# Optimization experiments

Hardware: AMD Instinct MI355X
Metric: run time of the kernel (lower is better)

The kernel has to match this reference:

```python
import jax, jax.numpy as jnp
import numpy as np

B, CQ, CK, CV, CO = 16, 256, 256, 256, 256
H, W = 80, 80          # query spatial size (P3-like)
KH, KW = 40, 40        # key/value spatial size (P4-like)
HEADS = 4
R2 = 2 * 2             # region_size ** 2
SCALE = 1.0 / np.float32(np.sqrt(CQ))


def conv1x1(x, w, b):
    # 1x1 conv == per-pixel linear map over channels
    return jnp.einsum('bchw,oc->bohw', x, w) + b[None, :, None, None]


def setup_inputs() -> dict:
    key = jax.random.key(0)
    ks = jax.random.split(key, 10)
    s = 0.05
    return {
        'query': jax.random.normal(ks[0], (B, CQ, H, W), jnp.float32),
        'key':   jax.random.normal(ks[1], (B, CK, KH, KW), jnp.float32),
        'wq': jax.random.normal(ks[2], (CQ, CQ), jnp.float32) * s,
        'bq': jax.random.normal(ks[3], (CQ,), jnp.float32) * s,
        'wk': jax.random.normal(ks[4], (CK, CK), jnp.float32) * s,
        'bk': jax.random.normal(ks[5], (CK,), jnp.float32) * s,
        'wv': jax.random.normal(ks[6], (CV, CV), jnp.float32) * s,
        'bv': jax.random.normal(ks[7], (CV,), jnp.float32) * s,
        'wo': jax.random.normal(ks[8], (CO, CV), jnp.float32) * s,
        'bo': jax.random.normal(ks[9], (CO,), jnp.float32) * s,
    }


def reference(query, key, wq, bq, wk, bk, wv, bv, wo, bo):
    # value defaults to key in the original module
    q = conv1x1(query, wq, bq)               # [B,CQ,H,W]
    k = conv1x1(key, wk, bk)                 # [B,CK,KH,KW]
    v = conv1x1(key, wv, bv)                 # [B,CV,KH,KW]

    b, cq, h, w = q.shape
    # All R2 'patches' in the source are the SAME interpolation (no offsets),
    # so compute it once; bilinear resize matches torch align_corners=False.
    ki = jax.image.resize(k, (b, k.shape[1], h, w), method='bilinear')
    vi = jax.image.resize(v, (b, v.shape[1], h, w), method='bilinear')

    q5 = q.reshape(b, HEADS, cq // HEADS, h, w)
    k5 = ki.reshape(b, HEADS, k.shape[1] // HEADS, h, w)
    v5 = vi.reshape(b, HEADS, v.shape[1] // HEADS, h, w)

    # per-region score; identical for every region patch
    score = jnp.einsum('bhcxy,bhcxy->bhxy', q5, k5) * SCALE     # [B,h,H,W]
    scores = jnp.broadcast_to(score[:, :, None], (b, HEADS, R2, h, w))
    # NOTE: original uses nn.Softmax(dim=3) -> normalizes over the H axis
    attn = jax.nn.softmax(scores, axis=3)                       # [B,h,R2,H,W]

    # out = sum over regions of attn * v (v identical across regions)
    out = jnp.einsum('bhrxy,bhcxy->bhcxy', attn, v5)            # [B,h,C/h,H,W]
    out = out.reshape(b, -1, h, w)                              # [B,CV,H,W]
    return conv1x1(out, wo, bo)                                 # [B,CO,H,W]
```

## Files before the change

kernel.cpp:

```cpp
#include <hip/hip_runtime.h>
#include <hip/hip_bf16.h>

typedef __bf16 bf16;
typedef __attribute__((ext_vector_type(4))) float f32x4;
typedef __attribute__((ext_vector_type(8))) __bf16 bf16x8;
typedef __attribute__((ext_vector_type(4))) __bf16 bf16x4;

static __device__ __forceinline__ void gl16(const void* g, void* l) {
  __builtin_amdgcn_global_load_lds((const __attribute__((address_space(1))) void*)g,
                                   (__attribute__((address_space(3))) void*)l, 16, 0, 0);
}
static __device__ __forceinline__ bf16x8 frag(const bf16* tile, int row, int kb) {
  return *(const bf16x8*)(tile + row * 64 + ((((kb) >> 3) ^ (row & 7)) << 3));
}

__global__ void wpre(const float* __restrict__ w0, const float* __restrict__ w1,
                     const float* __restrict__ w2, const float* __restrict__ w3,
                     bf16* __restrict__ dst) {
  const float* srcs[4] = {w0, w1, w2, w3};
  const float* s = srcs[blockIdx.y];
  bf16* d = dst + (size_t)blockIdx.y * 65536;
  int base = blockIdx.x * 2048 + threadIdx.x * 8;
  f32x4 a = *(const f32x4*)(s + base);
  f32x4 b = *(const f32x4*)(s + base + 4);
  bf16x8 v = {(bf16)a[0], (bf16)a[1], (bf16)a[2], (bf16)a[3],
              (bf16)b[0], (bf16)b[1], (bf16)b[2], (bf16)b[3]};
  *(bf16x8*)(d + base) = v;
}

__global__ __launch_bounds__(512, 1)
void qgemm_score(const float* __restrict__ query, const bf16* __restrict__ Wq,
                 const float* __restrict__ bq, const bf16* __restrict__ Kpm,
                 float* __restrict__ score) {
  __shared__ alignas(16) char smem[65536];
  const int t = threadIdx.x;
  const int b = blockIdx.z;
  const int m0 = blockIdx.x * 128;
  const int n0 = blockIdx.y * 128;
  const int w = t >> 6, l = t & 63;
  const int wr = w & 1, wc = w >> 1;
  const int lrow = l & 15, koff = (l >> 4) * 8;
  const int up = t & 31, uk = t >> 5;
  const float* actb = query + (size_t)b * 256 * 6400;

  f32x4 Ar[4];
  f32x4 acc[4][2];
#pragma unroll
  for (int i = 0; i < 4; ++i)
#pragma unroll
    for (int j = 0; j < 2; ++j) acc[i][j] = (f32x4){0.f, 0.f, 0.f, 0.f};

  auto Ab = [&](int buf) { return (bf16*)(smem + buf * 16384); };
  auto Bb = [&](int buf) { return (bf16*)(smem + 32768 + buf * 16384); };

  auto GLOADB = [&](int kt, int buf) {
    const int k0 = kt * 64;
#pragma unroll
    for (int call = 0; call < 2; ++call) {
      int idx = call * 512 + t;
      int row = idx >> 3, u = idx & 7;
      gl16(Wq + (size_t)(n0 + row) * 256 + k0 + ((u ^ (row & 7)) << 3), Bb(buf) + idx * 8);
    }
  };
  auto ALOAD = [&](int kt) {
    const int k0 = kt * 64;
    int ps = m0 + up * 4;
#pragma unroll
    for (int j = 0; j < 4; ++j)
      Ar[j] = *(const f32x4*)(actb + (size_t)(k0 + uk * 4 + j) * 6400 + ps);
  };
  auto ASTORE = [&](int buf) {
#pragma unroll
    for (int j = 0; j < 4; ++j) {
      int row = up * 4 + j;
      int cs = (uk * 4) ^ ((row & 7) << 3);
      bf16x4 v = {(bf16)Ar[0][j], (bf16)Ar[1][j], (bf16)Ar[2][j], (bf16)Ar[3][j]};
      *(bf16x4*)(Ab(buf) + row * 64 + cs) = v;
    }
  };
  auto COMPUTE = [&](int buf) {
#pragma unroll
    for (int kk = 0; kk < 2; ++kk) {
      const int kb = kk * 32 + koff;
      bf16x8 af[4], bv[2];
#pragma unroll
      for (int i = 0; i < 4; ++i) af[i] = frag(Ab(buf), wr * 64 + i * 16 + lrow, kb);
#pragma unroll
      for (int j = 0; j < 2; ++j) bv[j] = frag(Bb(buf), wc * 32 + j * 16 + lrow, kb);
#pragma unroll
      for (int i = 0; i < 4; ++i)
#pragma unroll
        for (int j = 0; j < 2; ++j)
          acc[i][j] = __builtin_amdgcn_mfma_f32_16x16x32_bf16(af[i], bv[j], acc[i][j], 0, 0, 0);
    }
  };

  GLOADB(0, 0);
  ALOAD(0);
  ASTORE(0);
  __syncthreads();
#pragma unroll
  for (int kt = 0; kt < 4; ++kt) {
    const int cur = kt & 1;
    if (kt < 3) { GLOADB(kt + 1, cur ^ 1); ALOAD(kt + 1); }
    __builtin_amdgcn_sched_barrier(0);
    COMPUTE(cur);
    if (kt < 3) ASTORE(cur ^ 1);
    __syncthreads();
  }

  bf16* Qs = (bf16*)smem;
#pragma unroll
  for (int mi = 0; mi < 4; ++mi) {
#pragma unroll
    for (int ni = 0; ni < 2; ++ni) {
      int ch = wc * 32 + ni * 16 + (l & 15);
      float bvf = bq[n0 + ch];
#pragma unroll
      for (int r = 0; r < 4; ++r) {
        int p = wr * 64 + mi * 16 + (l >> 4) * 4 + r;
        Qs[p * 136 + ch] = (bf16)(acc[mi][ni][r] + bvf);
      }
    }
  }
  __syncthreads();

  if (t < 256) {
    int pl = t & 127, hl = t >> 7;
    int hd = (n0 >> 6) + hl;
    int p = m0 + pl;
    int x = p / 80, y = p % 80;
    float cx = 0.5f * x - 0.25f;
    int ix = (int)floorf(cx);
    float wx1 = cx - ix;
    int x0 = ix < 0 ? 0 : ix, x1 = (ix + 1 > 39) ? 39 : ix + 1;
    float cy = 0.5f * y - 0.25f;
    int iy = (int)floorf(cy);
    float wy1 = cy - iy;
    int y0 = iy < 0 ? 0 : iy, y1 = (iy + 1 > 39) ? 39 : iy + 1;
    float w00 = (1.f - wx1) * (1.f - wy1), w01 = (1.f - wx1) * wy1;
    float w10 = wx1 * (1.f - wy1), w11 = wx1 * wy1;
    const bf16* k00 = Kpm + ((size_t)b * 1600 + x0 * 40 + y0) * 256 + hd * 64;
    const bf16* k01 = Kpm + ((size_t)b * 1600 + x0 * 40 + y1) * 256 + hd * 64;
    const bf16* k10 = Kpm + ((size_t)b * 1600 + x1 * 40 + y0) * 256 + hd * 64;
    const bf16* k11 = Kpm + ((size_t)b * 1600 + x1 * 40 + y1) * 256 + hd * 64;
    float dot = 0.f;
#pragma unroll
    for (int i = 0; i < 8; ++i) {
      bf16x8 qv = *(const bf16x8*)(Qs + pl * 136 + hl * 64 + i * 8);
      bf16x8 a = *(const bf16x8*)(k00 + i * 8);
      bf16x8 c = *(const bf16x8*)(k01 + i * 8);
      bf16x8 d = *(const bf16x8*)(k10 + i * 8);
      bf16x8 e = *(const bf16x8*)(k11 + i * 8);
#pragma unroll
      for (int j = 0; j < 8; ++j) {
        float kup = w00 * (float)a[j] + w01 * (float)c[j] + w10 * (float)d[j] + w11 * (float)e[j];
        dot += (float)qv[j] * kup;
      }
    }
    score[((size_t)b * 4 + hd) * 6400 + p] = dot * 0.0625f;
  }
}

__global__ __launch_bounds__(512, 1)
void kv_gemm(const float* __restrict__ key,
             const bf16* __restrict__ Wk, const float* __restrict__ bk, bf16* __restrict__ Kpm,
             const bf16* __restrict__ Wv, const float* __restrict__ bv, bf16* __restrict__ Vpm) {
  __shared__ alignas(16) char smem[65536];
  const int P = 1600;
  const int t = threadIdx.x;
  const int b = blockIdx.z;
  const int m0 = blockIdx.x * 128;
  const int sel = blockIdx.y >> 1;
  const int n0 = (blockIdx.y & 1) * 128;
  const bf16* W = sel ? Wv : Wk;
  const float* bias = sel ? bv : bk;
  bf16* out = sel ? Vpm : Kpm;
  const int w = t >> 6, l = t & 63;
  const int wr = w & 1, wc = w >> 1;
  const int lrow = l & 15, koff = (l >> 4) * 8;
  const int up = t & 31, uk = t >> 5;
  const float* actb = key + (size_t)b * 256 * P;

  f32x4 Ar[4];
  f32x4 acc[4][2];
#pragma unroll
  for (int i = 0; i < 4; ++i)
#pragma unroll
    for (int j = 0; j < 2; ++j) acc[i][j] = (f32x4){0.f, 0.f, 0.f, 0.f};

  auto Ab = [&](int buf) { return (bf16*)(smem + buf * 16384); };
  auto Bb = [&](int buf) { return (bf16*)(smem + 32768 + buf * 16384); };

  auto GLOADB = [&](int kt, int buf) {
    const int k0 = kt * 64;
#pragma unroll
    for (int call = 0; call < 2; ++call) {
      int idx = call * 512 + t;
      int row = idx >> 3, u = idx & 7;
      gl16(W + (size_t)(n0 + row) * 256 + k0 + ((u ^ (row & 7)) << 3), Bb(buf) + idx * 8);
    }
  };
  auto ALOAD = [&](int kt) {
    const int k0 = kt * 64;
    int ps = m0 + up * 4;
    if (ps > P - 4) ps = P - 4;
#pragma unroll
    for (int j = 0; j < 4; ++j)
      Ar[j] = *(const f32x4*)(actb + (size_t)(k0 + uk * 4 + j) * P + ps);
  };
  auto ASTORE = [&](int buf) {
#pragma unroll
    for (int j = 0; j < 4; ++j) {
      int row = up * 4 + j;
      int cs = (uk * 4) ^ ((row & 7) << 3);
      bf16x4 v = {(bf16)Ar[0][j], (bf16)Ar[1][j], (bf16)Ar[2][j], (bf16)Ar[3][j]};
      *(bf16x4*)(Ab(buf) + row * 64 + cs) = v;
    }
  };
  auto COMPUTE = [&](int buf) {
#pragma unroll
    for (int kk = 0; kk < 2; ++kk) {
      const int kb = kk * 32 + koff;
      bf16x8 af[4], bvv[2];
#pragma unroll
      for (int i = 0; i < 4; ++i) af[i] = frag(Ab(buf), wr * 64 + i * 16 + lrow, kb);
#pragma unroll
      for (int j = 0; j < 2; ++j) bvv[j] = frag(Bb(buf), wc * 32 + j * 16 + lrow, kb);
#pragma unroll
      for (int i = 0; i < 4; ++i)
#pragma unroll
        for (int j = 0; j < 2; ++j)
          acc[i][j] = __builtin_amdgcn_mfma_f32_16x16x32_bf16(af[i], bvv[j], acc[i][j], 0, 0, 0);
    }
  };

  GLOADB(0, 0);
  ALOAD(0);
  ASTORE(0);
  __syncthreads();
#pragma unroll
  for (int kt = 0; kt < 4; ++kt) {
    const int cur = kt & 1;
    if (kt < 3) { GLOADB(kt + 1, cur ^ 1); ALOAD(kt + 1); }
    __builtin_amdgcn_sched_barrier(0);
    COMPUTE(cur);
    if (kt < 3) ASTORE(cur ^ 1);
    __syncthreads();
  }

  bf16* Sc = (bf16*)smem;
#pragma unroll
  for (int mi = 0; mi < 4; ++mi) {
#pragma unroll
    for (int ni = 0; ni < 2; ++ni) {
      int ch = wc * 32 + ni * 16 + (l & 15);
      float bvf = bias[n0 + ch];
#pragma unroll
      for (int r = 0; r < 4; ++r) {
        int p = wr * 64 + mi * 16 + (l >> 4) * 4 + r;
        Sc[p * 136 + ch] = (bf16)(acc[mi][ni][r] + bvf);
      }
    }
  }
  __syncthreads();
  bf16* ob = out + (size_t)b * P * 256;
#pragma unroll
  for (int pass = 0; pass < 4; ++pass) {
    int unit = pass * 512 + t;
    int row = unit >> 4, cu = unit & 15;
    if (m0 + row < P) {
      bf16x8 v = *(const bf16x8*)(Sc + row * 136 + cu * 8);
      *(bf16x8*)(ob + (size_t)(m0 + row) * 256 + n0 + cu * 8) = v;
    }
  }
}

__global__ void smax_kernel(float* __restrict__ score) {
  __shared__ float s[6400];
  const int hd = blockIdx.x, b = blockIdx.y, t = threadIdx.x;
  float* buf = score + ((size_t)b * 4 + hd) * 6400;
  for (int i = t; i < 6400; i += 256) s[i] = buf[i];
  __syncthreads();
  if (t < 80) {
    const int y = t;
    float m = -1e30f;
    for (int x = 0; x < 80; ++x) m = fmaxf(m, s[x * 80 + y]);
    float sum = 0.f;
    for (int x = 0; x < 80; ++x) {
      float e = __expf(s[x * 80 + y] - m);
      s[x * 80 + y] = e;
      sum += e;
    }
    float inv = 4.0f / sum;
    for (int x = 0; x < 80; ++x) buf[x * 80 + y] = s[x * 80 + y] * inv;
  }
}

__global__ void outgen_kernel(const bf16* __restrict__ Vpm, const float* __restrict__ attn,
                              bf16* __restrict__ outpm) {
  __shared__ float Vx[40][256];
  __shared__ float at[4][80];
  const int x = blockIdx.x, b = blockIdx.y, t = threadIdx.x;

  float cx = 0.5f * x - 0.25f;
  int ix = (int)floorf(cx);
  float wx1 = cx - ix, wx0 = 1.f - wx1;
  int tx0 = ix < 0 ? 0 : ix, tx1 = (ix + 1 > 39) ? 39 : ix + 1;

  const bf16* r0 = Vpm + ((size_t)b * 1600 + tx0 * 40) * 256;
  const bf16* r1 = Vpm + ((size_t)b * 1600 + tx1 * 40) * 256;
  for (int ty = 0; ty < 40; ++ty)
    Vx[ty][t] = wx0 * (float)r0[ty * 256 + t] + wx1 * (float)r1[ty * 256 + t];
  for (int i = t; i < 320; i += 256) {
    int hd = i / 80, y = i % 80;
    at[hd][y] = attn[((size_t)b * 4 + hd) * 6400 + x * 80 + y];
  }
  __syncthreads();

  const int hd = t >> 6;
  bf16* ob = outpm + ((size_t)b * 6400 + x * 80) * 256;
  for (int y = 0; y < 80; ++y) {
    float cyv = 0.5f * y - 0.25f;
    int iy = (int)floorf(cyv);
    float wy1 = cyv - iy;
    int ty0 = iy < 0 ? 0 : iy, ty1 = (iy + 1 > 39) ? 39 : iy + 1;
    float v = (1.f - wy1) * Vx[ty0][t] + wy1 * Vx[ty1][t];
    ob[(size_t)y * 256 + t] = (bf16)(at[hd][y] * v);
  }
}

__global__ __launch_bounds__(512, 1)
void gemm_out(const bf16* __restrict__ act, const bf16* __restrict__ Wo,
              const float* __restrict__ bias, float* __restrict__ out) {
  __shared__ alignas(16) char smem[65536];
  const int t = threadIdx.x;
  const int b = blockIdx.z;
  const int m0 = blockIdx.x * 128;
  const int n0 = blockIdx.y * 128;
  const int w = t >> 6, l = t & 63;
  const int wr = w & 1, wc = w >> 1;
  const int lrow = l & 15, koff = (l >> 4) * 8;
  const bf16* actb = act + (size_t)b * 6400 * 256;

  f32x4 acc[4][2];
#pragma unroll
  for (int i = 0; i < 4; ++i)
#pragma unroll
    for (int j = 0; j < 2; ++j) acc[i][j] = (f32x4){0.f, 0.f, 0.f, 0.f};

  auto Ab = [&](int buf) { return (bf16*)(smem + buf * 16384); };
  auto Bb = [&](int buf) { return (bf16*)(smem + 32768 + buf * 16384); };

  auto GLOADS = [&](int kt, int buf) {
    const int k0 = kt * 64;
#pragma unroll
    for (int call = 0; call < 2; ++call) {
      int idx = call * 512 + t;
      int row = idx >> 3, u = idx & 7;
      gl16(actb + (size_t)(m0 + row) * 256 + k0 + ((u ^ (row & 7)) << 3), Ab(buf) + idx * 8);
      gl16(Wo + (size_t)(n0 + row) * 256 + k0 + ((u ^ (row & 7)) << 3), Bb(buf) + idx * 8);
    }
  };
  auto COMPUTE = [&](int buf) {
#pragma unroll
    for (int kk = 0; kk < 2; ++kk) {
      const int kb = kk * 32 + koff;
      bf16x8 af[4], bvv[2];
#pragma unroll
      for (int i = 0; i < 4; ++i) af[i] = frag(Ab(buf), wr * 64 + i * 16 + lrow, kb);
#pragma unroll
      for (int j = 0; j < 2; ++j) bvv[j] = frag(Bb(buf), wc * 32 + j * 16 + lrow, kb);
#pragma unroll
      for (int i = 0; i < 4; ++i)
#pragma unroll
        for (int j = 0; j < 2; ++j)
          acc[i][j] = __builtin_amdgcn_mfma_f32_16x16x32_bf16(af[i], bvv[j], acc[i][j], 0, 0, 0);
    }
  };

  GLOADS(0, 0);
  __syncthreads();
#pragma unroll
  for (int kt = 0; kt < 4; ++kt) {
    const int cur = kt & 1;
    if (kt < 3) GLOADS(kt + 1, cur ^ 1);
    __builtin_amdgcn_sched_barrier(0);
    COMPUTE(cur);
    __syncthreads();
  }

  float* ob = out + (size_t)b * 256 * 6400;
#pragma unroll
  for (int mi = 0; mi < 4; ++mi) {
    int pbase = m0 + wr * 64 + mi * 16 + (l >> 4) * 4;
#pragma unroll
    for (int ni = 0; ni < 2; ++ni) {
      int o_ = n0 + wc * 32 + ni * 16 + (l & 15);
      float bvf = bias[o_];
      f32x4 v = {acc[mi][ni][0] + bvf, acc[mi][ni][1] + bvf,
                 acc[mi][ni][2] + bvf, acc[mi][ni][3] + bvf};
      *(f32x4*)(ob + (size_t)o_ * 6400 + pbase) = v;
    }
  }
}

extern "C" void kernel_launch(void* const* d_in, const int* in_sizes, int n_in,
                              void* d_out, int out_size, void* d_ws, size_t ws_size,
                              hipStream_t stream) {
  const float* query = (const float*)d_in[0];
  const float* key   = (const float*)d_in[1];
  const float* wq    = (const float*)d_in[2];
  const float* bq    = (const float*)d_in[3];
  const float* wk    = (const float*)d_in[4];
  const float* bk    = (const float*)d_in[5];
  const float* wv    = (const float*)d_in[6];
  const float* bv    = (const float*)d_in[7];
  const float* wo    = (const float*)d_in[8];
  const float* bo    = (const float*)d_in[9];

  char* ws = (char*)d_ws;
  bf16*  outpm = (bf16*)(ws);
  bf16*  Kpm   = (bf16*)(ws + 52428800);
  bf16*  Vpm   = (bf16*)(ws + 65536000);
  float* score = (float*)(ws + 78643200);
  bf16*  Wb    = (bf16*)(ws + 85196800);
  bf16* wqb = Wb, *wkb = Wb + 65536, *wvb = Wb + 131072, *wob = Wb + 196608;

  wpre<<<dim3(32, 4), 256, 0, stream>>>(wq, wk, wv, wo, Wb);
  kv_gemm<<<dim3(13, 4, 16), 512, 0, stream>>>(key, wkb, bk, Kpm, wvb, bv, Vpm);
  qgemm_score<<<dim3(50, 2, 16), 512, 0, stream>>>(query, wqb, bq, Kpm, score);
  smax_kernel<<<dim3(4, 16), 256, 0, stream>>>(score);
  outgen_kernel<<<dim3(80, 16), 256, 0, stream>>>(Vpm, score, outpm);
  gemm_out<<<dim3(50, 2, 16), 512, 0, stream>>>(outpm, wob, bo, (float*)d_out);
}
```

Before: 179.6 us.

## Restructure Q-projection+score kernel to compute all 256 channels per 64-pixel tile

The Q projection kernel now tiles 64 pixels by all 256 output channels per block, so the query activation is read once instead of twice and every head's score is computed in one block. Weight fragments are loaded straight from global memory into registers instead of being staged through LDS, and the block shrinks to 256 threads with three blocks per CU targeted for occupancy. In exchange, each wave reads weights directly from global/L2 with no LDS reuse, and the accumulator tile per wave grows.

```diff
diff --git a/kernel.cpp b/kernel.cpp
--- a/kernel.cpp
+++ b/kernel.cpp
@@ -28,107 +28,100 @@
   *(bf16x8*)(d + base) = v;
 }
 
-__global__ __launch_bounds__(512, 1)
-void qgemm_score(const float* __restrict__ query, const bf16* __restrict__ Wq,
-                 const float* __restrict__ bq, const bf16* __restrict__ Kpm,
-                 float* __restrict__ score) {
-  __shared__ alignas(16) char smem[65536];
+__global__ __launch_bounds__(256, 3)
+void qscore(const float* __restrict__ query, const bf16* __restrict__ Wq,
+            const float* __restrict__ bq, const bf16* __restrict__ Kpm,
+            float* __restrict__ score) {
+  __shared__ alignas(16) char smem[64 * 264 * 2];
   const int t = threadIdx.x;
   const int b = blockIdx.z;
-  const int m0 = blockIdx.x * 128;
-  const int n0 = blockIdx.y * 128;
+  const int p0 = blockIdx.x * 64;
   const int w = t >> 6, l = t & 63;
-  const int wr = w & 1, wc = w >> 1;
-  const int lrow = l & 15, koff = (l >> 4) * 8;
-  const int up = t & 31, uk = t >> 5;
+  const int lrow = l & 15, ksel = l >> 4;
+  const int pq = t & 15, cq = t >> 4;
   const float* actb = query + (size_t)b * 256 * 6400;
 
+  auto Bt = [&](int buf) { return (bf16*)(smem + buf * 8192); };
+
   f32x4 Ar[4];
-  f32x4 acc[4][2];
-#pragma unroll
-  for (int i = 0; i < 4; ++i)
-#pragma unroll
-    for (int j = 0; j < 2; ++j) acc[i][j] = (f32x4){0.f, 0.f, 0.f, 0.f};
-
-  auto Ab = [&](int buf) { return (bf16*)(smem + buf * 16384); };
-  auto Bb = [&](int buf) { return (bf16*)(smem + 32768 + buf * 16384); };
-
-  auto GLOADB = [&](int kt, int buf) {
-    const int k0 = kt * 64;
-#pragma unroll
-    for (int call = 0; call < 2; ++call) {
-      int idx = call * 512 + t;
-      int row = idx >> 3, u = idx & 7;
-      gl16(Wq + (size_t)(n0 + row) * 256 + k0 + ((u ^ (row & 7)) << 3), Bb(buf) + idx * 8);
-    }
-  };
   auto ALOAD = [&](int kt) {
     const int k0 = kt * 64;
-    int ps = m0 + up * 4;
 #pragma unroll
     for (int j = 0; j < 4; ++j)
-      Ar[j] = *(const f32x4*)(actb + (size_t)(k0 + uk * 4 + j) * 6400 + ps);
+      Ar[j] = *(const f32x4*)(actb + (size_t)(k0 + cq * 4 + j) * 6400 + p0 + pq * 4);
   };
   auto ASTORE = [&](int buf) {
-#pragma unroll
-    for (int j = 0; j < 4; ++j) {
-      int row = up * 4 + j;
-      int cs = (uk * 4) ^ ((row & 7) << 3);
-      bf16x4 v = {(bf16)Ar[0][j], (bf16)Ar[1][j], (bf16)Ar[2][j], (bf16)Ar[3][j]};
-      *(bf16x4*)(Ab(buf) + row * 64 + cs) = v;
-    }
-  };
-  auto COMPUTE = [&](int buf) {
-#pragma unroll
-    for (int kk = 0; kk < 2; ++kk) {
-      const int kb = kk * 32 + koff;
-      bf16x8 af[4], bv[2];
-#pragma unroll
-      for (int i = 0; i < 4; ++i) af[i] = frag(Ab(buf), wr * 64 + i * 16 + lrow, kb);
-#pragma unroll
-      for (int j = 0; j < 2; ++j) bv[j] = frag(Bb(buf), wc * 32 + j * 16 + lrow, kb);
-#pragma unroll
-      for (int i = 0; i < 4; ++i)
-#pragma unroll
-        for (int j = 0; j < 2; ++j)
-          acc[i][j] = __builtin_amdgcn_mfma_f32_16x16x32_bf16(af[i], bv[j], acc[i][j], 0, 0, 0);
-    }
-  };
-
-  GLOADB(0, 0);
+    bf16* tile = Bt(buf);
+#pragma unroll
+    for (int e = 0; e < 4; ++e) {
+      int row = pq * 4 + e;
+      bf16x4 v = {(bf16)Ar[0][e], (bf16)Ar[1][e], (bf16)Ar[2][e], (bf16)Ar[3][e]};
+      *(bf16x4*)(tile + row * 64 + ((((cq >> 1) ^ (row & 7)) << 3) | ((cq & 1) << 2))) = v;
+    }
+  };
+
+  f32x4 acc[4][4];
+#pragma unroll
+  for (int i = 0; i < 4; ++i)
+#pragma unroll
+    for (int j = 0; j < 4; ++j) acc[i][j] = (f32x4){0.f, 0.f, 0.f, 0.f};
+
+  auto COMPUTE = [&](int kt, int buf) {
+    const int k0 = kt * 64;
+    bf16x8 af[4][2];
+#pragma unroll
+    for (int mi = 0; mi < 4; ++mi)
+#pragma unroll
+      for (int kk = 0; kk < 2; ++kk)
+        af[mi][kk] = *(const bf16x8*)(Wq + (size_t)(w * 64 + mi * 16 + lrow) * 256 +
+                                      k0 + kk * 32 + ksel * 8);
+    bf16x8 bv[4][2];
+#pragma unroll
+    for (int ni = 0; ni < 4; ++ni)
+#pragma unroll
+      for (int kk = 0; kk < 2; ++kk)
+        bv[ni][kk] = frag(Bt(buf), ni * 16 + lrow, kk * 32 + ksel * 8);
+#pragma unroll
+    for (int kk = 0; kk < 2; ++kk)
+#pragma unroll
+      for (int mi = 0; mi < 4; ++mi)
+#pragma unroll
+        for (int ni = 0; ni < 4; ++ni)
+          acc[mi][ni] = __builtin_amdgcn_mfma_f32_16x16x32_bf16(af[mi][kk], bv[ni][kk],
+                                                                acc[mi][ni], 0, 0, 0);
+  };
+
   ALOAD(0);
   ASTORE(0);
   __syncthreads();
 #pragma unroll
   for (int kt = 0; kt < 4; ++kt) {
-    const int cur = kt & 1;
-    if (kt < 3) { GLOADB(kt + 1, cur ^ 1); ALOAD(kt + 1); }
-    __builtin_amdgcn_sched_barrier(0);
-    COMPUTE(cur);
-    if (kt < 3) ASTORE(cur ^ 1);
+    if (kt < 3) ALOAD(kt + 1);
+    COMPUTE(kt, kt & 1);
+    if (kt < 3) ASTORE((kt + 1) & 1);
     __syncthreads();
   }
 
+  __syncthreads();
   bf16* Qs = (bf16*)smem;
 #pragma unroll
   for (int mi = 0; mi < 4; ++mi) {
 #pragma unroll
-    for (int ni = 0; ni < 2; ++ni) {
-      int ch = wc * 32 + ni * 16 + (l & 15);
-      float bvf = bq[n0 + ch];
-#pragma unroll
-      for (int r = 0; r < 4; ++r) {
-        int p = wr * 64 + mi * 16 + (l >> 4) * 4 + r;
-        Qs[p * 136 + ch] = (bf16)(acc[mi][ni][r] + bvf);
+    for (int r = 0; r < 4; ++r) {
+      int o = w * 64 + mi * 16 + ksel * 4 + r;
+      float bvf = bq[o];
+#pragma unroll
+      for (int ni = 0; ni < 4; ++ni) {
+        int px = ni * 16 + lrow;
+        Qs[px * 264 + o] = (bf16)(acc[mi][ni][r] + bvf);
       }
     }
   }
   __syncthreads();
 
-  if (t < 256) {
-    int pl = t & 127, hl = t >> 7;
-    int hd = (n0 >> 6) + hl;
-    int p = m0 + pl;
+  {
+    int pl = t & 63, hd = t >> 6;
+    int p = p0 + pl;
     int x = p / 80, y = p % 80;
     float cx = 0.5f * x - 0.25f;
     int ix = (int)floorf(cx);
@@ -147,7 +140,7 @@
     float dot = 0.f;
 #pragma unroll
     for (int i = 0; i < 8; ++i) {
-      bf16x8 qv = *(const bf16x8*)(Qs + pl * 136 + hl * 64 + i * 8);
+      bf16x8 qv = *(const bf16x8*)(Qs + pl * 264 + hd * 64 + i * 8);
       bf16x8 a = *(const bf16x8*)(k00 + i * 8);
       bf16x8 c = *(const bf16x8*)(k01 + i * 8);
       bf16x8 d = *(const bf16x8*)(k10 + i * 8);
@@ -221,8 +214,8 @@
   auto COMPUTE = [&](int buf) {
 #pragma unroll
     for (int kk = 0; kk < 2; ++kk) {
+      bf16x8 af[4], bvv[2];
       const int kb = kk * 32 + koff;
-      bf16x8 af[4], bvv[2];
 #pragma unroll
       for (int i = 0; i < 4; ++i) af[i] = frag(Ab(buf), wr * 64 + i * 16 + lrow, kb);
 #pragma unroll
@@ -365,8 +358,8 @@
   auto COMPUTE = [&](int buf) {
 #pragma unroll
     for (int kk = 0; kk < 2; ++kk) {
+      bf16x8 af[4], bvv[2];
       const int kb = kk * 32 + koff;
-      bf16x8 af[4], bvv[2];
 #pragma unroll
       for (int i = 0; i < 4; ++i) af[i] = frag(Ab(buf), wr * 64 + i * 16 + lrow, kb);
 #pragma unroll
@@ -429,7 +422,7 @@
 
   wpre<<<dim3(32, 4), 256, 0, stream>>>(wq, wk, wv, wo, Wb);
   kv_gemm<<<dim3(13, 4, 16), 512, 0, stream>>>(key, wkb, bk, Kpm, wvb, bv, Vpm);
-  qgemm_score<<<dim3(50, 2, 16), 512, 0, stream>>>(query, wqb, bq, Kpm, score);
+  qscore<<<dim3(100, 1, 16), 256, 0, stream>>>(query, wqb, bq, Kpm, score);
   smax_kernel<<<dim3(4, 16), 256, 0, stream>>>(score);
   outgen_kernel<<<dim3(80, 16), 256, 0, stream>>>(Vpm, score, outpm);
   gemm_out<<<dim3(50, 2, 16), 512, 0, stream>>>(outpm, wob, bo, (float*)d_out);
```

After: 172.9 us. 3.7% less time.
